# Performance work log

Hardware: AMD Instinct MI355X
Metric: run time of the kernel (lower is better)

Reference implementation:

```python
import jax, jax.numpy as jnp
import numpy as np

B, S, D, H, O = 4, 128, 768, 768, 2

def setup_inputs() -> dict:
    key = jax.random.key(0)
    ks = jax.random.split(key, 6)
    scale = 1.0 / np.sqrt(2 * D)
    return {
        "a": jax.random.normal(ks[0], (B, S, D), jnp.float32),
        "b": jax.random.normal(ks[1], (B, S, D), jnp.float32),
        "W1": jax.random.normal(ks[2], (2 * D, H), jnp.float32) * scale,
        "b1": jax.random.normal(ks[3], (H,), jnp.float32) * 0.01,
        "W2": jax.random.normal(ks[4], (H, O), jnp.float32) * (1.0 / np.sqrt(H)),
        "b2": jax.random.normal(ks[5], (O,), jnp.float32) * 0.01,
    }

def reference(a, b, W1, b1, W2, b2):
    # Pairwise concat [a_i ; b_j] followed by Linear(2D->H) is algebraically
    # identical to projecting a and b separately and broadcast-adding
    # (biaffine-style rewrite; same math as cat+matmul, less HBM traffic).
    d = a.shape[-1]
    ha = jnp.einsum('bsd,dh->bsh', a, W1[:d])        # (B, Sa, H)
    hb = jnp.einsum('btd,dh->bth', b, W1[d:])        # (B, Sb, H)
    h = jax.nn.relu(ha[:, :, None, :] + hb[:, None, :, :] + b1)  # (B, Sa, Sb, H)
    scores = jnp.einsum('bsth,ho->bsto', h, W2) + b2  # (B, Sa, Sb, O)
    return scores
```

## Files before the change

### kernel.cpp

```cpp
#include <hip/hip_runtime.h>
#include <hip/hip_fp16.h>


typedef __attribute__((ext_vector_type(2))) _Float16 half2t;
typedef __attribute__((ext_vector_type(8))) _Float16 half8t;
typedef __attribute__((ext_vector_type(4))) float floatx4;
typedef unsigned int uint;

__device__ __forceinline__ half2t pkrtz(float x, float y) {
    __fp16 r __attribute__((ext_vector_type(2))) = __builtin_amdgcn_cvt_pkrtz(x, y);
    half2t o; __builtin_memcpy(&o, &r, 4); return o;
}

__global__ __launch_bounds__(256) void gemm_kernel(
    const float* __restrict__ a, const float* __restrict__ bmat,
    const float* __restrict__ W1, const float* __restrict__ b1,
    const float* __restrict__ W2,
    ushort* __restrict__ Hf,
    uint* __restrict__ W2pk)
{
    const int which = blockIdx.z;
    const int n0 = blockIdx.x * 32;
    const int m0 = blockIdx.y * 32;
    const int t  = threadIdx.x;

    if (blockIdx.x == 0 && blockIdx.y == 0 && which == 0) {
#pragma unroll
        for (int j = t; j < 768; j += 256) {
            const int o  = (j >= 384) ? 1 : 0;
            const int h2 = j - o * 384;
            half2t pw = pkrtz(W2[4 * h2 + o], W2[4 * h2 + 2 + o]);
            uint u; __builtin_memcpy(&u, &pw, 4);
            W2pk[j] = u;
        }
    }

    __shared__ ushort As[2][32][72];
    __shared__ ushort Bs[2][32][72];

    const int arow = t >> 3;
    const int akc  = (t & 7) * 8;
    const float* __restrict__ Asrc = which ? bmat : a;
    const float* __restrict__ aptr = Asrc + (size_t)(m0 + arow) * 768 + akc;

    const int ncol = t & 31;
    const int kg   = (t >> 5) * 8;
    const float* __restrict__ bptr = W1 + (size_t)(which * 768 + kg) * 768 + n0 + ncol;

    const int lane = t & 63;
    const int w    = t >> 6;
    const int mh   = w >> 1;
    const int nh   = w & 1;
    const int lr   = lane & 15;
    const int lq   = lane >> 4;

    floatx4 acc = {0, 0, 0, 0};

    float4 a4[2];
    float  br[8];
    a4[0] = *(const float4*)(aptr);
    a4[1] = *(const float4*)(aptr + 4);
#pragma unroll
    for (int j = 0; j < 8; j++) br[j] = bptr[(size_t)j * 768];

    int p = 0;
    for (int kt = 0; kt < 768; kt += 64, p ^= 1) {
        float4 a4n[2];
        float  brn[8];
        if (kt + 64 < 768) {
            a4n[0] = *(const float4*)(aptr + kt + 64);
            a4n[1] = *(const float4*)(aptr + kt + 68);
#pragma unroll
            for (int j = 0; j < 8; j++)
                brn[j] = bptr[(size_t)(kt + 64 + j) * 768];
        }

        half2t ap[4];
        ap[0] = pkrtz(a4[0].x, a4[0].y);
        ap[1] = pkrtz(a4[0].z, a4[0].w);
        ap[2] = pkrtz(a4[1].x, a4[1].y);
        ap[3] = pkrtz(a4[1].z, a4[1].w);
        __builtin_memcpy(&As[p][arow][akc], ap, 16);
        half2t bp[4];
#pragma unroll
        for (int j = 0; j < 4; j++) bp[j] = pkrtz(br[2 * j], br[2 * j + 1]);
        __builtin_memcpy(&Bs[p][ncol][kg], bp, 16);

        __syncthreads();

#pragma unroll
        for (int h = 0; h < 2; h++) {
            const int kb = h * 32 + lq * 8;
            half8t afr, bfr;
            __builtin_memcpy(&afr, &As[p][mh * 16 + lr][kb], 16);
            __builtin_memcpy(&bfr, &Bs[p][nh * 16 + lr][kb], 16);
            acc = __builtin_amdgcn_mfma_f32_16x16x32_f16(afr, bfr, acc, 0, 0, 0);
        }

        a4[0] = a4n[0]; a4[1] = a4n[1];
#pragma unroll
        for (int j = 0; j < 8; j++) br[j] = brn[j];
    }

    const int ncolO = n0 + nh * 16 + lr;
    const float bias = which ? 0.f : b1[ncolO];
    ushort* __restrict__ dst = Hf + (size_t)which * 393216 + ncolO;
    const int rbase = m0 + mh * 16 + lq * 4;
#pragma unroll
    for (int r = 0; r < 4; r++) {
        _Float16 v = (_Float16)(acc[r] + bias);
        ushort u; __builtin_memcpy(&u, &v, 2);
        dst[(size_t)(rbase + r) * 768] = u;
    }
}

__global__ __launch_bounds__(256) void pair_kernel(
    const ushort* __restrict__ Hf, const uint* __restrict__ W2pk,
    const float* __restrict__ b2, float* __restrict__ out)
{
    const int bb = blockIdx.z >> 1;
    const int hh = blockIdx.z & 1;
    const int s0 = blockIdx.y * 16;
    const int t0 = blockIdx.x * 16;
    const int tid = threadIdx.x;

    __shared__ ushort hAs[16][392];
    __shared__ ushort hBs[16][392];

    const int hbase = hh * 384;
    const ushort* __restrict__ Asrc = Hf +          (size_t)(bb * 128 + s0) * 768 + hbase;
    const ushort* __restrict__ Bsrc = Hf + 393216 + (size_t)(bb * 128 + t0) * 768 + hbase;

#pragma unroll
    for (int i = 0; i < 3; i++) {
        const int c   = tid + i * 256;
        const int row = c / 48;
        const int col = (c % 48) * 8;
        *(uint4*)&hAs[row][col] = *(const uint4*)(Asrc + (size_t)row * 768 + col);
        *(uint4*)&hBs[row][col] = *(const uint4*)(Bsrc + (size_t)row * 768 + col);
    }
    __syncthreads();

    const int sl = tid >> 4;
    const int tl = tid & 15;
    const ushort* __restrict__ arow = &hAs[sl][0];
    const ushort* __restrict__ brow = &hBs[tl][0];
    const uint* __restrict__ w2o0 = W2pk +       hh * 192;
    const uint* __restrict__ w2o1 = W2pk + 384 + hh * 192;

    float acc0 = 0.f, acc1 = 0.f;
    const half2t zero = {(_Float16)0.f, (_Float16)0.f};

#pragma unroll 8
    for (int h8 = 0; h8 < 384; h8 += 8) {
        half2t pa[4], pb[4], w0[4], w1[4];
        __builtin_memcpy(pa, arow + h8, 16);
        __builtin_memcpy(pb, brow + h8, 16);
        __builtin_memcpy(w0, &w2o0[h8 / 2], 16);
        __builtin_memcpy(w1, &w2o1[h8 / 2], 16);
#pragma unroll
        for (int j = 0; j < 4; j++) {
            half2t s = pa[j] + pb[j];
            s = __builtin_elementwise_max(s, zero);
            acc0 = __builtin_amdgcn_fdot2(s, w0[j], acc0, false);
            acc1 = __builtin_amdgcn_fdot2(s, w1[j], acc1, false);
        }
    }

    if (hh == 0) { acc0 += b2[0]; acc1 += b2[1]; }
    const int sg = bb * 128 + s0 + sl;
    const int tg = t0 + tl;
    float* ob = &out[((size_t)sg * 128 + tg) * 2];
    unsafeAtomicAdd(ob,     acc0);
    unsafeAtomicAdd(ob + 1, acc1);
}

extern "C" void kernel_launch(void* const* d_in, const int* in_sizes, int n_in,
                              void* d_out, int out_size, void* d_ws, size_t ws_size,
                              hipStream_t stream) {
    const float* a  = (const float*)d_in[0];
    const float* b  = (const float*)d_in[1];
    const float* W1 = (const float*)d_in[2];
    const float* b1 = (const float*)d_in[3];
    const float* W2 = (const float*)d_in[4];
    const float* b2 = (const float*)d_in[5];
    float* out = (float*)d_out;

    ushort* Hf   = (ushort*)d_ws;
    uint*   W2pk = (uint*)((char*)d_ws + (2 << 20));

    gemm_kernel<<<dim3(24, 16, 2), 256, 0, stream>>>(a, b, W1, b1, W2, Hf, W2pk);
    pair_kernel<<<dim3(8, 8, 8), 256, 0, stream>>>(Hf, W2pk, b2, out);
}
```

Before: 83.74 us.

## Split pair kernel hidden dim eight ways and keep A rows in registers

The pair kernel now splits the hidden dimension into 8 chunks of 96 instead of 2 chunks of 384, which quadruples the grid so more blocks are resident. Each thread loads its own A row slice directly into registers rather than staging it in shared memory, and only the B tile goes through LDS. The cost is four times as many atomic adds to the output and redundant global reads of A rows across the 16 threads that share a row.

```diff
diff --git a/kernel.cpp b/kernel.cpp
--- a/kernel.cpp
+++ b/kernel.cpp
@@ -10,6 +10,9 @@
 __device__ __forceinline__ half2t pkrtz(float x, float y) {
     __fp16 r __attribute__((ext_vector_type(2))) = __builtin_amdgcn_cvt_pkrtz(x, y);
     half2t o; __builtin_memcpy(&o, &r, 4); return o;
+}
+__device__ __forceinline__ half2t h2cast(uint u) {
+    half2t o; __builtin_memcpy(&o, &u, 4); return o;
 }
 
 __global__ __launch_bounds__(256) void gemm_kernel(
@@ -118,49 +121,48 @@
     const ushort* __restrict__ Hf, const uint* __restrict__ W2pk,
     const float* __restrict__ b2, float* __restrict__ out)
 {
-    const int bb = blockIdx.z >> 1;
-    const int hh = blockIdx.z & 1;
+    const int bb = blockIdx.z >> 3;
+    const int hh = blockIdx.z & 7;
     const int s0 = blockIdx.y * 16;
     const int t0 = blockIdx.x * 16;
     const int tid = threadIdx.x;
+    const int sl = tid >> 4;
+    const int tl = tid & 15;
 
-    __shared__ ushort hAs[16][392];
-    __shared__ ushort hBs[16][392];
+    __shared__ ushort hBs[16][104];
 
-    const int hbase = hh * 384;
-    const ushort* __restrict__ Asrc = Hf +          (size_t)(bb * 128 + s0) * 768 + hbase;
+    const int hbase = hh * 96;
     const ushort* __restrict__ Bsrc = Hf + 393216 + (size_t)(bb * 128 + t0) * 768 + hbase;
+    if (tid < 192) {
+        const int row = tid / 12;
+        const int ch  = (tid % 12) * 8;
+        *(uint4*)&hBs[row][ch] = *(const uint4*)(Bsrc + (size_t)row * 768 + ch);
+    }
 
+    const ushort* __restrict__ Arow = Hf + (size_t)(bb * 128 + s0 + sl) * 768 + hbase;
+    uint4 areg[12];
 #pragma unroll
-    for (int i = 0; i < 3; i++) {
-        const int c   = tid + i * 256;
-        const int row = c / 48;
-        const int col = (c % 48) * 8;
-        *(uint4*)&hAs[row][col] = *(const uint4*)(Asrc + (size_t)row * 768 + col);
-        *(uint4*)&hBs[row][col] = *(const uint4*)(Bsrc + (size_t)row * 768 + col);
-    }
+    for (int i = 0; i < 12; i++) areg[i] = *(const uint4*)(Arow + i * 8);
+
     __syncthreads();
 
-    const int sl = tid >> 4;
-    const int tl = tid & 15;
-    const ushort* __restrict__ arow = &hAs[sl][0];
-    const ushort* __restrict__ brow = &hBs[tl][0];
-    const uint* __restrict__ w2o0 = W2pk +       hh * 192;
-    const uint* __restrict__ w2o1 = W2pk + 384 + hh * 192;
+    const uint* __restrict__ w2o0 = W2pk +       hh * 48;
+    const uint* __restrict__ w2o1 = W2pk + 384 + hh * 48;
 
     float acc0 = 0.f, acc1 = 0.f;
     const half2t zero = {(_Float16)0.f, (_Float16)0.f};
 
-#pragma unroll 8
-    for (int h8 = 0; h8 < 384; h8 += 8) {
-        half2t pa[4], pb[4], w0[4], w1[4];
-        __builtin_memcpy(pa, arow + h8, 16);
-        __builtin_memcpy(pb, brow + h8, 16);
+#pragma unroll
+    for (int h8 = 0; h8 < 96; h8 += 8) {
+        half2t pb[4], w0[4], w1[4];
+        __builtin_memcpy(pb, &hBs[tl][h8], 16);
         __builtin_memcpy(w0, &w2o0[h8 / 2], 16);
         __builtin_memcpy(w1, &w2o1[h8 / 2], 16);
+        const uint4 pa4 = areg[h8 / 8];
+        const uint pau[4] = {pa4.x, pa4.y, pa4.z, pa4.w};
 #pragma unroll
         for (int j = 0; j < 4; j++) {
-            half2t s = pa[j] + pb[j];
+            half2t s = h2cast(pau[j]) + pb[j];
             s = __builtin_elementwise_max(s, zero);
             acc0 = __builtin_amdgcn_fdot2(s, w0[j], acc0, false);
             acc1 = __builtin_amdgcn_fdot2(s, w1[j], acc1, false);
@@ -190,5 +192,5 @@
     uint*   W2pk = (uint*)((char*)d_ws + (2 << 20));
 
     gemm_kernel<<<dim3(24, 16, 2), 256, 0, stream>>>(a, b, W1, b1, W2, Hf, W2pk);
-    pair_kernel<<<dim3(8, 8, 8), 256, 0, stream>>>(Hf, W2pk, b2, out);
+    pair_kernel<<<dim3(8, 8, 32), 256, 0, stream>>>(Hf, W2pk, b2, out);
 }
```

Result: no change. 85.28 us (+1.8%).
